# Performance work log

Hardware: AMD Instinct MI355X
Metric: run time of the kernel (lower is better)

The kernel has to match this reference:

```python
import jax, jax.numpy as jnp
import numpy as np
import math

B, S, D, H = 8, 2048, 256, 8

def setup_inputs() -> dict:
    key = jax.random.key(0)
    k1, k2, k3 = jax.random.split(key, 3)
    e = jax.random.normal(k1, (B, S, D), dtype=jnp.float32)
    p = jax.random.normal(k2, (B, S + 1, D), dtype=jnp.float32)
    n_layer = 12
    W_o = jax.random.normal(k3, (D, D * H), dtype=jnp.float32) * (0.02 / math.sqrt(2 * n_layer))
    return {"e": e, "p": p, "W_o": W_o}

def reference(e, p, W_o):
    # e: [B,S,D], p: [B,S+1,D], W_o: [D, H*D] (nn.Linear weight)
    Bx, Sx, Dx = e.shape
    Hh = W_o.shape[1] // Dx
    # Original builds head-replicated Q=p, K=p[:-1], V=e; all heads compute
    # identical attention, so compute it once and tile for the W_o mix.
    q = p[:, 1:, :]   # rows 1..S of Q survive the [:, :, 1:, :] slice
    k = p[:, :-1, :]  # [B,S,D]
    scores = jnp.einsum('bqd,bkd->bqk', q, k) / math.sqrt(Dx)  # [B,S,S]
    scores = jnp.clip(scores, -10.0, 10.0)  # clamp happens BEFORE masking
    # Mask: tril(diag=-1) rows 1..S-1 plus an all-ones last row == standard
    # causal mask (col <= row) after the row slice.
    causal = jnp.tril(jnp.ones((Sx, Sx), dtype=bool))
    scores = jnp.where(causal[None, :, :], scores, -jnp.inf)
    attn = jax.nn.softmax(scores, axis=-1)
    y = jnp.einsum('bqk,bkd->bqd', attn, e)  # [B,S,D]
    # W_N diagonal matmul == per-row scale by 1/(i+1)
    row_scale = 1.0 / (jnp.arange(Sx, dtype=y.dtype) + 1.0)
    y = y * row_scale[None, :, None]
    y_cat = jnp.tile(y, (1, 1, Hh))  # heads are identical -> [B,S,H*D]
    out = y_cat @ W_o.T  # Linear(H*D -> D), no bias
    return out
```

## Files before the change

### kernel.cpp

```cpp
#include <hip/hip_runtime.h>


typedef __attribute__((ext_vector_type(8))) short short8;
typedef __attribute__((ext_vector_type(4))) float f32x4;

__device__ __forceinline__ unsigned short f2b(float x) {
  unsigned u = __builtin_bit_cast(unsigned, x);
  u = (u + 0x7fffu + ((u >> 16) & 1u)) >> 16;
  return (unsigned short)u;
}

#define GLOAD_LDS16(gp, lp)                                                                        \
  __builtin_amdgcn_global_load_lds((const __attribute__((address_space(1))) unsigned int*)(gp),    \
                                   (__attribute__((address_space(3))) unsigned int*)(lp), 16, 0, 0)

__global__ void cvt_p_kernel(const float* __restrict__ src, unsigned short* __restrict__ dst) {
  size_t t = (size_t)blockIdx.x * 256 + threadIdx.x;
  const float4* s = (const float4*)(src + t * 8);
  float4 a = s[0], b = s[1];
  short8 o;
  o[0] = (short)f2b(a.x); o[1] = (short)f2b(a.y); o[2] = (short)f2b(a.z); o[3] = (short)f2b(a.w);
  o[4] = (short)f2b(b.x); o[5] = (short)f2b(b.y); o[6] = (short)f2b(b.z); o[7] = (short)f2b(b.w);
  *(short8*)(dst + t * 8) = o;
}

__global__ void perm_e_kernel(const float* __restrict__ e, unsigned short* __restrict__ dst) {
  size_t t = (size_t)blockIdx.x * 256 + threadIdx.x;
  int lane = (int)(t & 63);
  int d0 = (int)((t >> 6) & 15);
  int kt = (int)((t >> 10) & 63);
  int b = (int)(t >> 16);
  int g = lane >> 4, l = lane & 15;
  const float* s = e + ((size_t)b * 2048 + kt * 32 + g * 8) * 256 + d0 * 16 + l;
  short8 o;
#pragma unroll
  for (int i = 0; i < 8; ++i) o[i] = (short)f2b(s[(size_t)i * 256]);
  *(short8*)(dst + t * 8) = o;
}

__global__ void fold_w_kernel(const float* __restrict__ w, unsigned short* __restrict__ dst) {
  int t = blockIdx.x * 256 + threadIdx.x;
  int lane = t & 63;
  int kc = (t >> 6) & 7;
  int d0 = t >> 9;
  int g = lane >> 4, l = lane & 15;
  const float* base = w + (size_t)(d0 * 16 + l) * 2048 + kc * 32 + g * 8;
  short8 o;
#pragma unroll
  for (int i = 0; i < 8; ++i) {
    float sum = 0.f;
#pragma unroll
    for (int h = 0; h < 8; ++h) sum += base[h * 256 + i];
    o[i] = (short)f2b(sum);
  }
  *(short8*)(dst + (size_t)t * 8) = o;
}

#define SMEM_BYTES 136320

__device__ __forceinline__ void stage_tiles(char* smem, int cur, int qh, int par, int kt, int b,
                                            int lane, const unsigned short* pbf,
                                            const unsigned short* eperm) {
  if (qh == 0) {
    const char* kb = (const char*)(pbf + ((size_t)b * 2049 + (size_t)kt * 32) * 256);
    char* dst = smem + cur * 65536 + par * 16384;
    int rlo = lane >> 5;
    int ci = (lane & 31) << 4;
#pragma unroll
    for (int j2 = 0; j2 < 16; ++j2) {
      int row = j2 * 2 + rlo;
      GLOAD_LDS16(kb + (row << 9) + (ci ^ ((row & 7) << 4)), dst + j2 * 1024);
    }
  } else {
    const char* eb = (const char*)(eperm + ((size_t)(b * 64 + kt)) * 8192);
    char* dst = smem + cur * 65536 + 32768 + par * 16384;
#pragma unroll
    for (int j2 = 0; j2 < 16; ++j2) GLOAD_LDS16(eb + j2 * 1024 + lane * 16, dst + j2 * 1024);
  }
}

__global__ __launch_bounds__(256, 1) void attn_main_kernel(const unsigned short* __restrict__ pbf,
                                                           const unsigned short* __restrict__ eperm,
                                                           const unsigned short* __restrict__ wfrag,
                                                           float* __restrict__ out) {
  __shared__ char smem[SMEM_BYTES];
  const int b = blockIdx.x & 7;
  const int pr = blockIdx.x >> 3;
  const int wave = threadIdx.x >> 6;
  const int lane = threadIdx.x & 63;
  const int qh = wave >> 1;
  const int par = wave & 1;
  const int g = lane >> 4;
  const int l = lane & 15;
  const f32x4 zero = {0.f, 0.f, 0.f, 0.f};

  for (int ti = 0; ti < 2; ++ti) {
    const int t = ti ? (63 - pr) : pr;
    const int qbase = t * 32 + qh * 16;

    short8 qf[8];
    {
      const unsigned short* qrow = pbf + ((size_t)b * 2049 + qbase + l + 1) * 256;
#pragma unroll
      for (int kc = 0; kc < 8; ++kc) qf[kc] = *(const short8*)(qrow + kc * 32 + g * 8);
    }
    f32x4 yacc[16];
#pragma unroll
    for (int i = 0; i < 16; ++i) yacc[i] = zero;
    float dsum[4] = {0.f, 0.f, 0.f, 0.f};

    const int nkt = t + 1;
    const int iters = (nkt + 1) >> 1;

    if (par < nkt) stage_tiles(smem, 0, qh, par, par, b, lane, pbf, eperm);
    __syncthreads();

    for (int it = 0; it < iters; ++it) {
      const int cur = it & 1;
      const int ktn = 2 * (it + 1) + par;
      if (it + 1 < iters && ktn < nkt)
        stage_tiles(smem, cur ^ 1, qh, par, ktn, b, lane, pbf, eperm);

      const int kt = 2 * it + par;
      if (kt < nkt) {
        const char* kbuf = smem + cur * 65536 + par * 16384;
        const char* ebuf = kbuf + 32768;
        f32x4 sacc[2];
        sacc[0] = zero;
        sacc[1] = zero;
#pragma unroll
        for (int kc = 0; kc < 8; ++kc) {
#pragma unroll
          for (int n0 = 0; n0 < 2; ++n0) {
            const int row = n0 * 16 + l;
            short8 bf =
                *(const short8*)(kbuf + row * 512 + ((kc * 64 + g * 16) ^ ((row & 7) << 4)));
            sacc[n0] = __builtin_amdgcn_mfma_f32_16x16x32_bf16(qf[kc], bf, sacc[n0], 0, 0, 0);
          }
        }
        unsigned short* pp = (unsigned short*)(smem + 131072 + wave * 1280);
#pragma unroll
        for (int n0 = 0; n0 < 2; ++n0) {
          const int kg = kt * 32 + n0 * 16 + l;
#pragma unroll
          for (int j = 0; j < 4; ++j) {
            float s = sacc[n0][j] * 0.0625f;
            s = fminf(fmaxf(s, -10.f), 10.f);
            const int qg = qbase + g * 4 + j;
            float w = (kg <= qg) ? __expf(s) : 0.f;
            dsum[j] += w;
            pp[(g * 4 + j) * 40 + n0 * 16 + l] = f2b(w);
          }
        }
        short8 af = *(const short8*)((const unsigned short*)pp + l * 40 + g * 8);
#pragma unroll
        for (int d0 = 0; d0 < 16; ++d0) {
          short8 ef = *(const short8*)(ebuf + d0 * 1024 + lane * 16);
          yacc[d0] = __builtin_amdgcn_mfma_f32_16x16x32_bf16(af, ef, yacc[d0], 0, 0, 0);
        }
      }
      __syncthreads();
    }

#pragma unroll
    for (int j = 0; j < 4; ++j) {
      float v = dsum[j];
      v += __shfl_xor(v, 1);
      v += __shfl_xor(v, 2);
      v += __shfl_xor(v, 4);
      v += __shfl_xor(v, 8);
      dsum[j] = v;
    }

    float* yc = (float*)smem + qh * (16 * 257);
    float* dc = (float*)(smem + 136192) + qh * 16;
    if (par == 1) {
#pragma unroll
      for (int d0 = 0; d0 < 16; ++d0)
#pragma unroll
        for (int j = 0; j < 4; ++j) yc[(g * 4 + j) * 257 + d0 * 16 + l] = yacc[d0][j];
      if (l == 0) {
#pragma unroll
        for (int j = 0; j < 4; ++j) dc[g * 4 + j] = dsum[j];
      }
    }
    __syncthreads();
    unsigned short* py = (unsigned short*)(smem + 65536) + qh * (16 * 264);
    if (par == 0) {
      float inv[4];
#pragma unroll
      for (int j = 0; j < 4; ++j) {
        float dtot = dsum[j] + dc[g * 4 + j];
        const int qg = qbase + g * 4 + j;
        inv[j] = 1.f / (dtot * (float)(qg + 1));
      }
#pragma unroll
      for (int d0 = 0; d0 < 16; ++d0)
#pragma unroll
        for (int j = 0; j < 4; ++j)
          py[(g * 4 + j) * 264 + d0 * 16 + l] =
              f2b((yacc[d0][j] + yc[(g * 4 + j) * 257 + d0 * 16 + l]) * inv[j]);
    }
    __syncthreads();

    {
      f32x4 oacc[8];
#pragma unroll
      for (int i = 0; i < 8; ++i) oacc[i] = zero;
#pragma unroll
      for (int kc = 0; kc < 8; ++kc) {
        short8 af2 = *(const short8*)(py + l * 264 + kc * 32 + g * 8);
#pragma unroll
        for (int dd = 0; dd < 8; ++dd) {
          const int d0 = par * 8 + dd;
          short8 wf = *(const short8*)(wfrag + ((size_t)(d0 * 8 + kc) * 64 + lane) * 8);
          oacc[dd] = __builtin_amdgcn_mfma_f32_16x16x32_bf16(af2, wf, oacc[dd], 0, 0, 0);
        }
      }
#pragma unroll
      for (int dd = 0; dd < 8; ++dd) {
#pragma unroll
        for (int j = 0; j < 4; ++j) {
          const int qg = qbase + g * 4 + j;
          const int d = (par * 8 + dd) * 16 + l;
          out[((size_t)b * 2048 + qg) * 256 + d] = oacc[dd][j];
        }
      }
    }
    __syncthreads();
  }
}

extern "C" void kernel_launch(void* const* d_in, const int* in_sizes, int n_in, void* d_out,
                              int out_size, void* d_ws, size_t ws_size, hipStream_t stream) {
  (void)in_sizes; (void)n_in; (void)out_size; (void)ws_size;
  const float* e = (const float*)d_in[0];
  const float* p = (const float*)d_in[1];
  const float* Wo = (const float*)d_in[2];
  float* out = (float*)d_out;

  unsigned short* pbf = (unsigned short*)d_ws;
  unsigned short* eperm = (unsigned short*)((char*)d_ws + 8392704);
  unsigned short* wfrag = (unsigned short*)((char*)d_ws + 16781312);

  hipLaunchKernelGGL(cvt_p_kernel, dim3(2049), dim3(256), 0, stream, p, pbf);
  hipLaunchKernelGGL(perm_e_kernel, dim3(2048), dim3(256), 0, stream, e, eperm);
  hipLaunchKernelGGL(fold_w_kernel, dim3(32), dim3(256), 0, stream, Wo, wfrag);
  hipLaunchKernelGGL(attn_main_kernel, dim3(256), dim3(256), 0, stream, pbf, eperm, wfrag, out);
}
```

Before: 166.9 us.

## Split attention into 16-row query blocks with 4-way key split across waves

The main kernel now launches 1024 blocks, each handling 16 query rows. Its four waves split the key tiles round-robin and reduce their partial outputs through LDS, where before 256 blocks each processed two 32-row tiles. K and E fragments are read straight from global memory instead of being double-buffered into LDS with async loads. LDS use drops enough to allow 4 blocks per CU, raising occupancy and load balance at the cost of losing LDS reuse and adding a serialized cross-wave reduction. The folded W_o is stored row-major rather than in fragment order.

```diff
diff --git a/kernel.cpp b/kernel.cpp
--- a/kernel.cpp
+++ b/kernel.cpp
@@ -9,10 +9,6 @@
   u = (u + 0x7fffu + ((u >> 16) & 1u)) >> 16;
   return (unsigned short)u;
 }
-
-#define GLOAD_LDS16(gp, lp)                                                                        \
-  __builtin_amdgcn_global_load_lds((const __attribute__((address_space(1))) unsigned int*)(gp),    \
-                                   (__attribute__((address_space(3))) unsigned int*)(lp), 16, 0, 0)
 
 __global__ void cvt_p_kernel(const float* __restrict__ src, unsigned short* __restrict__ dst) {
   size_t t = (size_t)blockIdx.x * 256 + threadIdx.x;
@@ -39,195 +35,166 @@
 }
 
 __global__ void fold_w_kernel(const float* __restrict__ w, unsigned short* __restrict__ dst) {
-  int t = blockIdx.x * 256 + threadIdx.x;
-  int lane = t & 63;
-  int kc = (t >> 6) & 7;
-  int d0 = t >> 9;
-  int g = lane >> 4, l = lane & 15;
-  const float* base = w + (size_t)(d0 * 16 + l) * 2048 + kc * 32 + g * 8;
-  short8 o;
-#pragma unroll
-  for (int i = 0; i < 8; ++i) {
-    float sum = 0.f;
-#pragma unroll
-    for (int h = 0; h < 8; ++h) sum += base[h * 256 + i];
-    o[i] = (short)f2b(sum);
-  }
-  *(short8*)(dst + (size_t)t * 8) = o;
-}
-
-#define SMEM_BYTES 136320
-
-__device__ __forceinline__ void stage_tiles(char* smem, int cur, int qh, int par, int kt, int b,
-                                            int lane, const unsigned short* pbf,
-                                            const unsigned short* eperm) {
-  if (qh == 0) {
-    const char* kb = (const char*)(pbf + ((size_t)b * 2049 + (size_t)kt * 32) * 256);
-    char* dst = smem + cur * 65536 + par * 16384;
-    int rlo = lane >> 5;
-    int ci = (lane & 31) << 4;
-#pragma unroll
-    for (int j2 = 0; j2 < 16; ++j2) {
-      int row = j2 * 2 + rlo;
-      GLOAD_LDS16(kb + (row << 9) + (ci ^ ((row & 7) << 4)), dst + j2 * 1024);
-    }
-  } else {
-    const char* eb = (const char*)(eperm + ((size_t)(b * 64 + kt)) * 8192);
-    char* dst = smem + cur * 65536 + 32768 + par * 16384;
-#pragma unroll
-    for (int j2 = 0; j2 < 16; ++j2) GLOAD_LDS16(eb + j2 * 1024 + lane * 16, dst + j2 * 1024);
-  }
-}
-
-__global__ __launch_bounds__(256, 1) void attn_main_kernel(const unsigned short* __restrict__ pbf,
+  int d = blockIdx.x;
+  int c = threadIdx.x;
+  const float* row = w + (size_t)d * 2048 + c;
+  float s = 0.f;
+#pragma unroll
+  for (int h = 0; h < 8; ++h) s += row[h * 256];
+  dst[d * 256 + c] = f2b(s);
+}
+
+#define SMEM_BYTES 25088
+
+__global__ __launch_bounds__(256, 4) void attn_main_kernel(const unsigned short* __restrict__ pbf,
                                                            const unsigned short* __restrict__ eperm,
-                                                           const unsigned short* __restrict__ wfrag,
+                                                           const unsigned short* __restrict__ wsum,
                                                            float* __restrict__ out) {
   __shared__ char smem[SMEM_BYTES];
   const int b = blockIdx.x & 7;
-  const int pr = blockIdx.x >> 3;
+  const int j0 = blockIdx.x >> 3;
+  const int t16 = (j0 < 64) ? j0 : 191 - j0;
+  const int qbase = t16 * 16;
+  const int nkt = (t16 >> 1) + 1;
   const int wave = threadIdx.x >> 6;
   const int lane = threadIdx.x & 63;
-  const int qh = wave >> 1;
-  const int par = wave & 1;
   const int g = lane >> 4;
   const int l = lane & 15;
   const f32x4 zero = {0.f, 0.f, 0.f, 0.f};
 
-  for (int ti = 0; ti < 2; ++ti) {
-    const int t = ti ? (63 - pr) : pr;
-    const int qbase = t * 32 + qh * 16;
-
-    short8 qf[8];
-    {
-      const unsigned short* qrow = pbf + ((size_t)b * 2049 + qbase + l + 1) * 256;
-#pragma unroll
-      for (int kc = 0; kc < 8; ++kc) qf[kc] = *(const short8*)(qrow + kc * 32 + g * 8);
-    }
-    f32x4 yacc[16];
-#pragma unroll
-    for (int i = 0; i < 16; ++i) yacc[i] = zero;
-    float dsum[4] = {0.f, 0.f, 0.f, 0.f};
-
-    const int nkt = t + 1;
-    const int iters = (nkt + 1) >> 1;
-
-    if (par < nkt) stage_tiles(smem, 0, qh, par, par, b, lane, pbf, eperm);
-    __syncthreads();
-
-    for (int it = 0; it < iters; ++it) {
-      const int cur = it & 1;
-      const int ktn = 2 * (it + 1) + par;
-      if (it + 1 < iters && ktn < nkt)
-        stage_tiles(smem, cur ^ 1, qh, par, ktn, b, lane, pbf, eperm);
-
-      const int kt = 2 * it + par;
-      if (kt < nkt) {
-        const char* kbuf = smem + cur * 65536 + par * 16384;
-        const char* ebuf = kbuf + 32768;
-        f32x4 sacc[2];
-        sacc[0] = zero;
-        sacc[1] = zero;
-#pragma unroll
-        for (int kc = 0; kc < 8; ++kc) {
-#pragma unroll
-          for (int n0 = 0; n0 < 2; ++n0) {
-            const int row = n0 * 16 + l;
-            short8 bf =
-                *(const short8*)(kbuf + row * 512 + ((kc * 64 + g * 16) ^ ((row & 7) << 4)));
-            sacc[n0] = __builtin_amdgcn_mfma_f32_16x16x32_bf16(qf[kc], bf, sacc[n0], 0, 0, 0);
-          }
-        }
-        unsigned short* pp = (unsigned short*)(smem + 131072 + wave * 1280);
-#pragma unroll
-        for (int n0 = 0; n0 < 2; ++n0) {
-          const int kg = kt * 32 + n0 * 16 + l;
-#pragma unroll
-          for (int j = 0; j < 4; ++j) {
-            float s = sacc[n0][j] * 0.0625f;
-            s = fminf(fmaxf(s, -10.f), 10.f);
-            const int qg = qbase + g * 4 + j;
-            float w = (kg <= qg) ? __expf(s) : 0.f;
-            dsum[j] += w;
-            pp[(g * 4 + j) * 40 + n0 * 16 + l] = f2b(w);
-          }
-        }
-        short8 af = *(const short8*)((const unsigned short*)pp + l * 40 + g * 8);
-#pragma unroll
-        for (int d0 = 0; d0 < 16; ++d0) {
-          short8 ef = *(const short8*)(ebuf + d0 * 1024 + lane * 16);
-          yacc[d0] = __builtin_amdgcn_mfma_f32_16x16x32_bf16(af, ef, yacc[d0], 0, 0, 0);
-        }
+  short8 qf[8];
+  {
+    const unsigned short* qrow = pbf + ((size_t)b * 2049 + qbase + l + 1) * 256;
+#pragma unroll
+    for (int kc = 0; kc < 8; ++kc) qf[kc] = *(const short8*)(qrow + kc * 32 + g * 8);
+  }
+
+  f32x4 yacc[16];
+#pragma unroll
+  for (int i = 0; i < 16; ++i) yacc[i] = zero;
+  float dsum[4] = {0.f, 0.f, 0.f, 0.f};
+
+  unsigned short* pp = (unsigned short*)(smem + 16384 + wave * 1280);
+  const unsigned short* kpool = pbf + (size_t)b * 2049 * 256;
+  const unsigned short* epool = eperm + (size_t)b * 64 * 8192 + (size_t)lane * 8;
+
+  for (int kt = wave; kt < nkt; kt += 4) {
+    f32x4 sacc0 = zero, sacc1 = zero;
+    const unsigned short* kb = kpool + (size_t)kt * 32 * 256;
+#pragma unroll
+    for (int kc = 0; kc < 8; ++kc) {
+      short8 k0 = *(const short8*)(kb + (size_t)l * 256 + kc * 32 + g * 8);
+      short8 k1 = *(const short8*)(kb + (size_t)(16 + l) * 256 + kc * 32 + g * 8);
+      sacc0 = __builtin_amdgcn_mfma_f32_16x16x32_bf16(qf[kc], k0, sacc0, 0, 0, 0);
+      sacc1 = __builtin_amdgcn_mfma_f32_16x16x32_bf16(qf[kc], k1, sacc1, 0, 0, 0);
+    }
+#pragma unroll
+    for (int n0 = 0; n0 < 2; ++n0) {
+      const int kg = kt * 32 + n0 * 16 + l;
+      const f32x4 sv = n0 ? sacc1 : sacc0;
+#pragma unroll
+      for (int jj = 0; jj < 4; ++jj) {
+        float s = sv[jj] * 0.0625f;
+        s = fminf(fmaxf(s, -10.f), 10.f);
+        const int qg = qbase + g * 4 + jj;
+        float w = (kg <= qg) ? __expf(s) : 0.f;
+        dsum[jj] += w;
+        pp[(g * 4 + jj) * 40 + n0 * 16 + l] = f2b(w);
       }
-      __syncthreads();
-    }
-
-#pragma unroll
-    for (int j = 0; j < 4; ++j) {
-      float v = dsum[j];
-      v += __shfl_xor(v, 1);
-      v += __shfl_xor(v, 2);
-      v += __shfl_xor(v, 4);
-      v += __shfl_xor(v, 8);
-      dsum[j] = v;
-    }
-
-    float* yc = (float*)smem + qh * (16 * 257);
-    float* dc = (float*)(smem + 136192) + qh * 16;
-    if (par == 1) {
-#pragma unroll
-      for (int d0 = 0; d0 < 16; ++d0)
-#pragma unroll
-        for (int j = 0; j < 4; ++j) yc[(g * 4 + j) * 257 + d0 * 16 + l] = yacc[d0][j];
-      if (l == 0) {
-#pragma unroll
-        for (int j = 0; j < 4; ++j) dc[g * 4 + j] = dsum[j];
+    }
+    short8 af = *(const short8*)((const unsigned short*)pp + l * 40 + g * 8);
+    const unsigned short* eb = epool + (size_t)kt * 8192;
+#pragma unroll
+    for (int d0 = 0; d0 < 16; ++d0) {
+      short8 ef = *(const short8*)(eb + d0 * 512);
+      yacc[d0] = __builtin_amdgcn_mfma_f32_16x16x32_bf16(af, ef, yacc[d0], 0, 0, 0);
+    }
+  }
+
+#pragma unroll
+  for (int jj = 0; jj < 4; ++jj) {
+    float v = dsum[jj];
+    v += __shfl_xor(v, 1);
+    v += __shfl_xor(v, 2);
+    v += __shfl_xor(v, 4);
+    v += __shfl_xor(v, 8);
+    dsum[jj] = v;
+  }
+  float* dbuf = (float*)(smem + 24832);
+  if (wave != 0 && l == 0) {
+#pragma unroll
+    for (int jj = 0; jj < 4; ++jj) dbuf[(wave - 1) * 16 + g * 4 + jj] = dsum[jj];
+  }
+
+  f32x4* bufv = (f32x4*)smem;
+  __syncthreads();
+  if (wave == 1) {
+#pragma unroll
+    for (int d0 = 0; d0 < 16; ++d0) bufv[d0 * 64 + lane] = yacc[d0];
+  }
+  __syncthreads();
+  if (wave == 0) {
+#pragma unroll
+    for (int d0 = 0; d0 < 16; ++d0) yacc[d0] += bufv[d0 * 64 + lane];
+  }
+  __syncthreads();
+  if (wave == 2) {
+#pragma unroll
+    for (int d0 = 0; d0 < 16; ++d0) bufv[d0 * 64 + lane] = yacc[d0];
+  }
+  __syncthreads();
+  if (wave == 0) {
+#pragma unroll
+    for (int d0 = 0; d0 < 16; ++d0) yacc[d0] += bufv[d0 * 64 + lane];
+  }
+  __syncthreads();
+  if (wave == 3) {
+#pragma unroll
+    for (int d0 = 0; d0 < 16; ++d0) bufv[d0 * 64 + lane] = yacc[d0];
+  }
+  __syncthreads();
+  unsigned short* py = (unsigned short*)(smem + 16384);
+  if (wave == 0) {
+    float inv[4];
+#pragma unroll
+    for (int jj = 0; jj < 4; ++jj) {
+      float dtot = dsum[jj] + dbuf[g * 4 + jj] + dbuf[16 + g * 4 + jj] + dbuf[32 + g * 4 + jj];
+      const int qg = qbase + g * 4 + jj;
+      inv[jj] = 1.f / (dtot * (float)(qg + 1));
+    }
+#pragma unroll
+    for (int d0 = 0; d0 < 16; ++d0) {
+      f32x4 yt = yacc[d0] + bufv[d0 * 64 + lane];
+#pragma unroll
+      for (int jj = 0; jj < 4; ++jj)
+        py[(g * 4 + jj) * 264 + d0 * 16 + l] = f2b(yt[jj] * inv[jj]);
+    }
+  }
+  __syncthreads();
+
+  {
+    f32x4 oacc[4];
+#pragma unroll
+    for (int i = 0; i < 4; ++i) oacc[i] = zero;
+#pragma unroll
+    for (int kc = 0; kc < 8; ++kc) {
+      short8 a2 = *(const short8*)(py + l * 264 + kc * 32 + g * 8);
+#pragma unroll
+      for (int dd = 0; dd < 4; ++dd) {
+        short8 wf =
+            *(const short8*)(wsum + (size_t)((wave * 4 + dd) * 16 + l) * 256 + kc * 32 + g * 8);
+        oacc[dd] = __builtin_amdgcn_mfma_f32_16x16x32_bf16(a2, wf, oacc[dd], 0, 0, 0);
       }
     }
-    __syncthreads();
-    unsigned short* py = (unsigned short*)(smem + 65536) + qh * (16 * 264);
-    if (par == 0) {
-      float inv[4];
-#pragma unroll
-      for (int j = 0; j < 4; ++j) {
-        float dtot = dsum[j] + dc[g * 4 + j];
-        const int qg = qbase + g * 4 + j;
-        inv[j] = 1.f / (dtot * (float)(qg + 1));
+#pragma unroll
+    for (int dd = 0; dd < 4; ++dd) {
+#pragma unroll
+      for (int jj = 0; jj < 4; ++jj) {
+        const int qg = qbase + g * 4 + jj;
+        const int d = (wave * 4 + dd) * 16 + l;
+        out[((size_t)b * 2048 + qg) * 256 + d] = oacc[dd][jj];
       }
-#pragma unroll
-      for (int d0 = 0; d0 < 16; ++d0)
-#pragma unroll
-        for (int j = 0; j < 4; ++j)
-          py[(g * 4 + j) * 264 + d0 * 16 + l] =
-              f2b((yacc[d0][j] + yc[(g * 4 + j) * 257 + d0 * 16 + l]) * inv[j]);
-    }
-    __syncthreads();
-
-    {
-      f32x4 oacc[8];
-#pragma unroll
-      for (int i = 0; i < 8; ++i) oacc[i] = zero;
-#pragma unroll
-      for (int kc = 0; kc < 8; ++kc) {
-        short8 af2 = *(const short8*)(py + l * 264 + kc * 32 + g * 8);
-#pragma unroll
-        for (int dd = 0; dd < 8; ++dd) {
-          const int d0 = par * 8 + dd;
-          short8 wf = *(const short8*)(wfrag + ((size_t)(d0 * 8 + kc) * 64 + lane) * 8);
-          oacc[dd] = __builtin_amdgcn_mfma_f32_16x16x32_bf16(af2, wf, oacc[dd], 0, 0, 0);
-        }
-      }
-#pragma unroll
-      for (int dd = 0; dd < 8; ++dd) {
-#pragma unroll
-        for (int j = 0; j < 4; ++j) {
-          const int qg = qbase + g * 4 + j;
-          const int d = (par * 8 + dd) * 16 + l;
-          out[((size_t)b * 2048 + qg) * 256 + d] = oacc[dd][j];
-        }
-      }
-    }
-    __syncthreads();
+    }
   }
 }
 
@@ -241,10 +208,10 @@
 
   unsigned short* pbf = (unsigned short*)d_ws;
   unsigned short* eperm = (unsigned short*)((char*)d_ws + 8392704);
-  unsigned short* wfrag = (unsigned short*)((char*)d_ws + 16781312);
+  unsigned short* wsum = (unsigned short*)((char*)d_ws + 16781312);
 
   hipLaunchKernelGGL(cvt_p_kernel, dim3(2049), dim3(256), 0, stream, p, pbf);
   hipLaunchKernelGGL(perm_e_kernel, dim3(2048), dim3(256), 0, stream, e, eperm);
-  hipLaunchKernelGGL(fold_w_kernel, dim3(32), dim3(256), 0, stream, Wo, wfrag);
-  hipLaunchKernelGGL(attn_main_kernel, dim3(256), dim3(256), 0, stream, pbf, eperm, wfrag, out);
-}
+  hipLaunchKernelGGL(fold_w_kernel, dim3(256), dim3(256), 0, stream, Wo, wsum);
+  hipLaunchKernelGGL(attn_main_kernel, dim3(1024), dim3(256), 0, stream, pbf, eperm, wsum, out);
+}
```

Measured after the change: 229.8 us. 1.38x slower.
